# Kernel optimization log

Hardware: AMD Instinct MI355X
Metric: run time of the kernel (lower is better)

## Reference

```python
import jax, jax.numpy as jnp
import numpy as np

# 24 directional shifts (dy, dx): out[h,w] = in[h-dy, w-dx], zero elsewhere.
SHIFTS = [(0,1),(0,-1),(1,0),(-1,0),(1,1),(-1,-1),(1,-1),(-1,1),
          (0,2),(0,-2),(2,0),(-2,0),(2,2),(-2,-2),(2,-2),(-2,2),
          (2,1),(1,2),(2,-1),(1,-2),(-2,1),(-1,2),(-2,-1),(-1,-2)]

def shift2d(xg, dy, dx):
    B, G, H, W = xg.shape
    pt, pb = max(dy,0), max(-dy,0)
    pl, pr = max(dx,0), max(-dx,0)
    xp = jnp.pad(xg, ((0,0),(0,0),(pt,pb),(pl,pr)))
    return xp[:, :, pb:pb+H, pr:pr+W]

def mul_shift(x4, gamma=1.0/24.0):
    B, C, H, W = x4.shape
    g = int(C * gamma)
    parts = [shift2d(x4[:, i*g:(i+1)*g], dy, dx) for i, (dy, dx) in enumerate(SHIFTS)]
    parts.append(x4[:, 24*g:])
    return jnp.concatenate(parts, axis=1)

def zigzag_indices(h, w, start='top-left', direction='horizontal'):
    if start == 'top-left':   row_start, col_start, row_step, col_step = 0, 0, 1, 1
    elif start == 'top-right': row_start, col_start, row_step, col_step = 0, w-1, 1, -1
    elif start == 'bottom-left': row_start, col_start, row_step, col_step = h-1, 0, -1, 1
    else:                     row_start, col_start, row_step, col_step = h-1, w-1, -1, -1
    idx = []
    for i in range(h):
        r = row_start + row_step * i
        if direction == 'horizontal':
            cols = range(w) if r % 2 == 0 else range(w-1, -1, -1)
            idx += [r * w + c for c in cols]
        else:
            cc = col_start + col_step * i
            rows = range(h) if cc % 2 == 0 else range(h-1, -1, -1)
            idx += [rr * w + cc for rr in rows]
    return np.asarray(idx, dtype=np.int32)

def wkv(w, u, k, v):
    """Numerically stable RWKV WKV recurrence. w,u:(C,) k,v:(B,T,C) -> (B,T,C)."""
    B, T, C = k.shape
    def step(carry, kv):
        p, q, o = carry
        kt, vt = kv
        no = jnp.maximum(o, u + kt)
        A = jnp.exp(o - no); Bc = jnp.exp(u + kt - no)
        y = (A * p + Bc * vt) / (A * q + Bc)
        no2 = jnp.maximum(w + o, kt)
        A2 = jnp.exp(w + o - no2); B2 = jnp.exp(kt - no2)
        return (A2 * p + B2 * vt, A2 * q + B2, no2), y
    init = (jnp.zeros((B, C), k.dtype), jnp.zeros((B, C), k.dtype),
            jnp.full((B, C), -1e38, k.dtype))
    _, ys = jax.lax.scan(step, init, (jnp.swapaxes(k, 0, 1), jnp.swapaxes(v, 0, 1)))
    return jnp.swapaxes(ys, 0, 1)

def setup_inputs() -> dict:
    key = jax.random.key(0)
    ks = jax.random.split(key, 8)
    B, H, W, C = 8, 64, 64, 768
    scale = 0.02
    return {
        'x': jax.random.normal(ks[0], (B, H*W, C), jnp.float32),
        'key_w': jax.random.normal(ks[1], (C, C), jnp.float32) * scale,
        'value_w': jax.random.normal(ks[2], (C, C), jnp.float32) * scale,
        'receptance_w': jax.random.normal(ks[3], (C, C), jnp.float32) * scale,
        'output_w': jax.random.normal(ks[4], (C, C), jnp.float32) * scale,
        'spatial_decay': jax.random.normal(ks[5], (2, C), jnp.float32),
        'spatial_first': jax.random.normal(ks[6], (2, C), jnp.float32),
        'h': H, 'w': W,
    }

def reference(x, key_w, value_w, receptance_w, output_w, spatial_decay, spatial_first, h, w):
    B, T, C = x.shape
    # layer_id=0 -> scheme ('top-left','horizontal')
    order = jnp.asarray(zigzag_indices(h, w, 'top-left', 'horizontal'))
    inv = jnp.argsort(order)
    # jit_func: mul_shift in (B,C,H,W), zigzag reorder along T, projections
    x4 = jnp.transpose(x.reshape(B, h, w, C), (0, 3, 1, 2))
    x4 = mul_shift(x4)
    xs = jnp.transpose(x4.reshape(B, C, T)[:, :, order], (0, 2, 1))  # (B,T,C)
    k = xs @ key_w.T
    v = xs @ value_w.T
    sr = jax.nn.sigmoid(xs @ receptance_w.T)
    # recurrence j=0
    v = wkv(spatial_decay[0] / T, spatial_first[0] / T, k, v)
    # recurrence j=1: zigzag-permute, WKV, inverse-permute (horizontal -> same grid)
    k2 = k[:, order]
    v2 = v[:, order]
    v2 = wkv(spatial_decay[1] / T, spatial_first[1] / T, k2, v2)
    v = v2[:, inv]
    return (sr * v) @ output_w.T
```

## Files before the change

### kernel.cpp

```cpp
#include <hip/hip_runtime.h>
#include <hip/hip_bf16.h>
#include <hip/hip_fp16.h>

#define T_SEQ 4096
#define CDIM  768
#define BDIM  8
#define MROWS (BDIM * T_SEQ)
#define NKVR  (3 * CDIM)
#define CHL   32
#define NCH   (T_SEQ / CHL)
#define BC    (BDIM * CDIM)
#define BC2   (BC / 2)
#define CD2   (CDIM / 2)

typedef __attribute__((ext_vector_type(8))) short   short8;
typedef __attribute__((ext_vector_type(4))) float   floatx4;
typedef unsigned short ushort_t;
typedef unsigned int   uint_t;

__device__ __forceinline__ ushort_t f2b(float f) {
    __hip_bfloat16 h = __float2bfloat16(f);
    return *(ushort_t*)&h;
}
__device__ __forceinline__ float b2f(ushort_t s) {
    __hip_bfloat16 h;
    *(ushort_t*)&h = s;
    return __bfloat162float(h);
}
__device__ __forceinline__ ushort_t f2h(float f) {
    __half h = __float2half(f);
    return *(ushort_t*)&h;
}
__device__ __forceinline__ float h2f(ushort_t s) {
    __half h;
    *(ushort_t*)&h = s;
    return __half2float(h);
}

__device__ __forceinline__ void gload_lds16(const void* g, void* l) {
    __builtin_amdgcn_global_load_lds(
        (const __attribute__((address_space(1))) void*)g,
        (__attribute__((address_space(3))) void*)l, 16, 0, 0);
}

__constant__ int c_dy[24] = {0,0,1,-1,1,-1,1,-1,0,0,2,-2,2,-2,2,-2,2,1,2,1,-2,-1,-2,-1};
__constant__ int c_dx[24] = {1,-1,0,0,1,-1,-1,1,2,-2,0,0,2,-2,-2,2,1,2,-1,-2,1,2,-1,-2};

__global__ void cvt_weights(const float* __restrict__ kw, const float* __restrict__ vw,
                            const float* __restrict__ rw, const float* __restrict__ ow,
                            ushort_t* __restrict__ wkvr, ushort_t* __restrict__ wo) {
    int i = blockIdx.x * 256 + threadIdx.x;
    if (i < CDIM * CDIM) {
        wkvr[i]                   = f2b(kw[i]);
        wkvr[i + CDIM * CDIM]     = f2b(vw[i]);
        wkvr[i + 2 * CDIM * CDIM] = f2b(rw[i]);
        wo[i]                     = f2b(ow[i]);
    }
}

__global__ void shift_zigzag(const float* __restrict__ x, ushort_t* __restrict__ xs) {
    size_t i = (size_t)blockIdx.x * 256 + threadIdx.x;
    int c8 = (int)(i % (CDIM / 8)) * 8;
    size_t bt = i / (CDIM / 8);
    int tz = (int)(bt % T_SEQ);
    int b  = (int)(bt / T_SEQ);
    int r = tz >> 6, pos = tz & 63;
    int xcol = (r & 1) ? (63 - pos) : pos;
    int g = c8 >> 5;
    int ys = r - c_dy[g];
    int xsrc = xcol - c_dx[g];
    float4 v0 = {0.f, 0.f, 0.f, 0.f}, v1 = {0.f, 0.f, 0.f, 0.f};
    if ((unsigned)ys < 64u && (unsigned)xsrc < 64u) {
        const float* src = x + ((size_t)b * T_SEQ + (size_t)(ys * 64 + xsrc)) * CDIM + c8;
        v0 = *(const float4*)(src);
        v1 = *(const float4*)(src + 4);
    }
    short8 o;
    o[0] = (short)f2b(v0.x); o[1] = (short)f2b(v0.y);
    o[2] = (short)f2b(v0.z); o[3] = (short)f2b(v0.w);
    o[4] = (short)f2b(v1.x); o[5] = (short)f2b(v1.y);
    o[6] = (short)f2b(v1.z); o[7] = (short)f2b(v1.w);
    *(short8*)(xs + bt * CDIM + c8) = o;
}

template <int MODE, int NB>
__device__ __forceinline__ void gemm_body(
    const ushort_t* __restrict__ A, const ushort_t* __restrict__ Bw,
    ushort_t* __restrict__ kbuf, ushort_t* __restrict__ vbuf,
    ushort_t* __restrict__ out_sr, float* __restrict__ out_f) {
    __shared__ ushort_t As[128 * 64];
    __shared__ ushort_t Bs[128 * 64];
    const int p    = blockIdx.x;
    const int xcd  = p & 7;
    const int s    = p >> 3;
    const int mb   = xcd + 8 * (s / NB);
    const int nb   = s % NB;
    const int m0   = mb * 128;
    const int n0   = nb * 128;
    const int t    = threadIdx.x;
    const int lane = t & 63;
    const int wv   = t >> 6;
    const int wm   = (wv & 1) * 64;
    const int wn   = (wv >> 1) * 64;
    const int srow = t >> 3;
    const int sch  = t & 7;
    const int l15  = lane & 15;
    const int l4   = lane >> 4;

    floatx4 acc[4][4];
#pragma unroll
    for (int i = 0; i < 4; i++)
#pragma unroll
        for (int j = 0; j < 4; j++) acc[i][j] = (floatx4){0.f, 0.f, 0.f, 0.f};

    for (int kk = 0; kk < CDIM; kk += 64) {
        __syncthreads();
#pragma unroll
        for (int j = 0; j < 4; j++) {
            const int rowA = 32 * j + srow;
            const int gc   = sch ^ (rowA & 7);
            gload_lds16(A  + (size_t)(m0 + rowA) * CDIM + kk + gc * 8,
                        (void*)(As + j * 2048 + t * 8));
            gload_lds16(Bw + (size_t)(n0 + rowA) * CDIM + kk + gc * 8,
                        (void*)(Bs + j * 2048 + t * 8));
        }
        __syncthreads();
#pragma unroll
        for (int k2 = 0; k2 < 2; k2++) {
            short8 af[4], bfv[4];
#pragma unroll
            for (int mi = 0; mi < 4; mi++) {
                int ra = wm + mi * 16 + l15;
                int c  = k2 * 4 + l4;
                af[mi] = *(const short8*)(As + ra * 64 + ((c ^ (ra & 7)) << 3));
            }
#pragma unroll
            for (int ni = 0; ni < 4; ni++) {
                int rb = wn + ni * 16 + l15;
                int c  = k2 * 4 + l4;
                bfv[ni] = *(const short8*)(Bs + rb * 64 + ((c ^ (rb & 7)) << 3));
            }
#pragma unroll
            for (int mi = 0; mi < 4; mi++)
#pragma unroll
                for (int ni = 0; ni < 4; ni++)
                    acc[mi][ni] = __builtin_amdgcn_mfma_f32_16x16x32_bf16(
                        af[mi], bfv[ni], acc[mi][ni], 0, 0, 0);
        }
    }

    const int region = (MODE == 0) ? (nb / 6) : 0;
    const int ncb = n0 - region * CDIM;
#pragma unroll
    for (int mi = 0; mi < 4; mi++) {
#pragma unroll
        for (int ni = 0; ni < 4; ni++) {
            int nc = ncb + wn + ni * 16 + l15;
#pragma unroll
            for (int r = 0; r < 4; r++) {
                int mg = m0 + wm + mi * 16 + l4 * 4 + r;
                float val = acc[mi][ni][r];
                if (MODE == 0) {
                    if (region == 0)
                        kbuf[(size_t)mg * CDIM + nc] = f2h(val);
                    else if (region == 1)
                        vbuf[(size_t)mg * CDIM + nc] = f2h(val);
                    else
                        out_sr[(size_t)mg * CDIM + nc] =
                            f2b(1.0f / (1.0f + __expf(-val)));
                } else {
                    out_f[(size_t)mg * CDIM + (n0 + wn + ni * 16 + l15)] = val;
                }
            }
        }
    }
}

__global__ __launch_bounds__(256, 3) void gemm_kvr(
    const ushort_t* __restrict__ A, const ushort_t* __restrict__ Bw,
    ushort_t* __restrict__ kbuf, ushort_t* __restrict__ vbuf,
    ushort_t* __restrict__ out_sr) {
    gemm_body<0, 18>(A, Bw, kbuf, vbuf, out_sr, nullptr);
}

__global__ __launch_bounds__(256, 3) void gemm_out(
    const ushort_t* __restrict__ A, const ushort_t* __restrict__ Bw,
    float* __restrict__ out_f) {
    gemm_body<1, 6>(A, Bw, nullptr, nullptr, nullptr, out_f);
}


__global__ __launch_bounds__(256) void wkv_chunk_sum0(
    const ushort_t* __restrict__ kb, const ushort_t* __restrict__ vb,
    const float* __restrict__ sd,
    float* __restrict__ sumP, float* __restrict__ sumQ, float* __restrict__ sumO) {
    int gid = blockIdx.x * 256 + threadIdx.x;
    int bc2 = gid % BC2;
    int ch  = gid / BC2;
    int b = bc2 / CD2, cp = (bc2 % CD2) * 2;
    const float w0 = sd[cp]     * (1.0f / (float)T_SEQ);
    const float w1 = sd[cp + 1] * (1.0f / (float)T_SEQ);
    const size_t base = ((size_t)b * T_SEQ + ch * CHL) * CDIM + cp;
    const uint_t* kp = (const uint_t*)(kb + base);
    const uint_t* vp = (const uint_t*)(vb + base);
    float p0 = 0.f, q0 = 0.f, o0 = -1e38f;
    float p1 = 0.f, q1 = 0.f, o1 = -1e38f;
#pragma unroll 8
    for (int i = 0; i < CHL; i++) {
        uint_t ku = kp[(size_t)i * CD2], vu = vp[(size_t)i * CD2];
        float k0 = h2f((ushort_t)(ku & 0xffff)), k1 = h2f((ushort_t)(ku >> 16));
        float v0 = h2f((ushort_t)(vu & 0xffff)), v1 = h2f((ushort_t)(vu >> 16));
        float wo0 = w0 + o0, wo1 = w1 + o1;
        float n0_ = fmaxf(wo0, k0), n1_ = fmaxf(wo1, k1);
        float A0 = __expf(wo0 - n0_), B0 = __expf(k0 - n0_);
        float A1 = __expf(wo1 - n1_), B1 = __expf(k1 - n1_);
        p0 = A0 * p0 + B0 * v0;  q0 = A0 * q0 + B0;  o0 = n0_;
        p1 = A1 * p1 + B1 * v1;  q1 = A1 * q1 + B1;  o1 = n1_;
    }
    size_t idx = (size_t)ch * BC + (size_t)b * CDIM + cp;
    *(float2*)(sumP + idx) = make_float2(p0, p1);
    *(float2*)(sumQ + idx) = make_float2(q0, q1);
    *(float2*)(sumO + idx) = make_float2(o0, o1);
}

__global__ __launch_bounds__(256) void wkv_chunk_scan(
    const float* __restrict__ sumP, const float* __restrict__ sumQ,
    const float* __restrict__ sumO,
    float* __restrict__ inP, float* __restrict__ inQ, float* __restrict__ inO,
    const float* __restrict__ sd, int pass) {
    int bc = blockIdx.x * 256 + threadIdx.x;
    if (bc >= BC) return;
    int c = bc % CDIM;
    const float w = sd[pass * CDIM + c] * (1.0f / (float)T_SEQ);
    const float Lw = w * (float)CHL;
    float p = 0.f, q = 0.f, o = -1e38f;
#pragma unroll 4
    for (int ch = 0; ch < NCH; ch++) {
        size_t idx = (size_t)ch * BC + bc;
        inP[idx] = p; inQ[idx] = q; inO[idx] = o;
        float Pc = sumP[idx], Qc = sumQ[idx], Oc = sumO[idx];
        float ow_ = o + Lw;
        float no = fmaxf(ow_, Oc);
        float e1 = __expf(ow_ - no), e2 = __expf(Oc - no);
        p = e1 * p + e2 * Pc;
        q = e1 * q + e2 * Qc;
        o = no;
    }
}

__global__ __launch_bounds__(256) void wkv_replay0_sum1(
    const ushort_t* __restrict__ kb, ushort_t* __restrict__ vb,
    const float* __restrict__ sd, const float* __restrict__ sf,
    const float* __restrict__ inP, const float* __restrict__ inQ,
    const float* __restrict__ inO,
    float* __restrict__ sumP, float* __restrict__ sumQ, float* __restrict__ sumO) {
    int gid = blockIdx.x * 256 + threadIdx.x;
    int bc2 = gid % BC2;
    int ch  = gid / BC2;
    int b = bc2 / CD2, cp = (bc2 % CD2) * 2;
    const float w10 = sd[cp]     * (1.0f / (float)T_SEQ);
    const float w11 = sd[cp + 1] * (1.0f / (float)T_SEQ);
    const float u10 = sf[cp]     * (1.0f / (float)T_SEQ);
    const float u11 = sf[cp + 1] * (1.0f / (float)T_SEQ);
    const size_t base = ((size_t)b * T_SEQ + ch * CHL) * CDIM + cp;
    const uint_t* kp = (const uint_t*)(kb + base);
    uint_t* vp = (uint_t*)(vb + base);
    size_t idx = (size_t)ch * BC + (size_t)b * CDIM + cp;
    float2 pin = *(const float2*)(inP + idx);
    float2 qin = *(const float2*)(inQ + idx);
    float2 oin = *(const float2*)(inO + idx);
    float p0 = pin.x, q0 = qin.x, o0 = oin.x;
    float p1 = pin.y, q1 = qin.y, o1 = oin.y;
    uint_t ku_[CHL];
    uint_t yu_[CHL];
#pragma unroll
    for (int i = 0; i < CHL; i++) {
        uint_t ku = kp[(size_t)i * CD2];
        uint_t vu = vp[(size_t)i * CD2];
        ku_[i] = ku;
        float k0 = h2f((ushort_t)(ku & 0xffff)), k1 = h2f((ushort_t)(ku >> 16));
        float v0 = h2f((ushort_t)(vu & 0xffff)), v1 = h2f((ushort_t)(vu >> 16));
        float uk0 = u10 + k0;
        float no0 = fmaxf(o0, uk0);
        float Ae0 = __expf(o0 - no0), Be0 = __expf(uk0 - no0);
        float y0 = (Ae0 * p0 + Be0 * v0) / (Ae0 * q0 + Be0);
        float wo0 = w10 + o0;
        float nn0 = fmaxf(wo0, k0);
        float A20 = __expf(wo0 - nn0), B20 = __expf(k0 - nn0);
        p0 = A20 * p0 + B20 * v0;  q0 = A20 * q0 + B20;  o0 = nn0;
        float uk1 = u11 + k1;
        float no1 = fmaxf(o1, uk1);
        float Ae1 = __expf(o1 - no1), Be1 = __expf(uk1 - no1);
        float y1 = (Ae1 * p1 + Be1 * v1) / (Ae1 * q1 + Be1);
        float wo1 = w11 + o1;
        float nn1 = fmaxf(wo1, k1);
        float A21 = __expf(wo1 - nn1), B21 = __expf(k1 - nn1);
        p1 = A21 * p1 + B21 * v1;  q1 = A21 * q1 + B21;  o1 = nn1;
        uint_t yu = (uint_t)f2h(y0) | ((uint_t)f2h(y1) << 16);
        yu_[i] = yu;
        vp[(size_t)i * CD2] = yu;
    }
    const float w20 = sd[CDIM + cp]     * (1.0f / (float)T_SEQ);
    const float w21 = sd[CDIM + cp + 1] * (1.0f / (float)T_SEQ);
    float p20 = 0.f, q20 = 0.f, o20 = -1e38f;
    float p21 = 0.f, q21 = 0.f, o21 = -1e38f;
#define P2STEP(I)                                                              \
    {                                                                          \
        uint_t ku = ku_[(I)], yu = yu_[(I)];                                   \
        float k0 = h2f((ushort_t)(ku & 0xffff)), k1 = h2f((ushort_t)(ku >> 16)); \
        float y0 = h2f((ushort_t)(yu & 0xffff)), y1 = h2f((ushort_t)(yu >> 16)); \
        float wo0 = w20 + o20, wo1 = w21 + o21;                                \
        float nn0 = fmaxf(wo0, k0), nn1 = fmaxf(wo1, k1);                      \
        float A20 = __expf(wo0 - nn0), B20 = __expf(k0 - nn0);                 \
        float A21 = __expf(wo1 - nn1), B21 = __expf(k1 - nn1);                 \
        p20 = A20 * p20 + B20 * y0;  q20 = A20 * q20 + B20;  o20 = nn0;        \
        p21 = A21 * p21 + B21 * y1;  q21 = A21 * q21 + B21;  o21 = nn1;        \
    }
    if (((ch >> 1) & 1) == 0) {
#pragma unroll
        for (int j = 0; j < CHL; j++) P2STEP(j)
    } else {
#pragma unroll
        for (int j = 0; j < CHL; j++) P2STEP(CHL - 1 - j)
    }
#undef P2STEP
    size_t idx2 = (size_t)((ch & 2) ? (ch ^ 1) : ch) * BC + (size_t)b * CDIM + cp;
    *(float2*)(sumP + idx2) = make_float2(p20, p21);
    *(float2*)(sumQ + idx2) = make_float2(q20, q21);
    *(float2*)(sumO + idx2) = make_float2(o20, o21);
}

__global__ __launch_bounds__(256) void wkv_replay1(
    const ushort_t* __restrict__ kb, const ushort_t* __restrict__ vb,
    const ushort_t* __restrict__ srb, ushort_t* __restrict__ a2,
    const float* __restrict__ sd, const float* __restrict__ sf,
    const float* __restrict__ inP, const float* __restrict__ inQ,
    const float* __restrict__ inO) {
    int gid = blockIdx.x * 256 + threadIdx.x;
    int bc2 = gid % BC2;
    int ch  = gid / BC2;
    int b = bc2 / CD2, cp = (bc2 % CD2) * 2;
    const float w0 = sd[CDIM + cp]     * (1.0f / (float)T_SEQ);
    const float w1 = sd[CDIM + cp + 1] * (1.0f / (float)T_SEQ);
    const float u0 = sf[CDIM + cp]     * (1.0f / (float)T_SEQ);
    const float u1 = sf[CDIM + cp + 1] * (1.0f / (float)T_SEQ);
    size_t base = (size_t)b * T_SEQ * CDIM + cp;
    size_t idx = (size_t)ch * BC + (size_t)b * CDIM + cp;
    float2 pin = *(const float2*)(inP + idx);
    float2 qin = *(const float2*)(inQ + idx);
    float2 oin = *(const float2*)(inO + idx);
    float p0 = pin.x, q0 = qin.x, o0 = oin.x;
    float p1 = pin.y, q1 = qin.y, o1 = oin.y;
    const int r = ch >> 1;
    const int pos0 = (ch & 1) * CHL;
#pragma unroll 8
    for (int i = 0; i < CHL; i++) {
        int pos = pos0 + i;
        int col = (r & 1) ? (63 - pos) : pos;
        size_t off = base + (size_t)(r * 64 + col) * CDIM;
        uint_t ku = *(const uint_t*)(kb + off);
        uint_t vu = *(const uint_t*)(vb + off);
        uint_t su = *(const uint_t*)(srb + off);
        float k0 = h2f((ushort_t)(ku & 0xffff)), k1 = h2f((ushort_t)(ku >> 16));
        float v0 = h2f((ushort_t)(vu & 0xffff)), v1 = h2f((ushort_t)(vu >> 16));
        float uk0 = u0 + k0;
        float no0 = fmaxf(o0, uk0);
        float Ae0 = __expf(o0 - no0), Be0 = __expf(uk0 - no0);
        float y0 = (Ae0 * p0 + Be0 * v0) / (Ae0 * q0 + Be0);
        float wo0 = w0 + o0;
        float nn0 = fmaxf(wo0, k0);
        float A20 = __expf(wo0 - nn0), B20 = __expf(k0 - nn0);
        p0 = A20 * p0 + B20 * v0;  q0 = A20 * q0 + B20;  o0 = nn0;
        float uk1 = u1 + k1;
        float no1 = fmaxf(o1, uk1);
        float Ae1 = __expf(o1 - no1), Be1 = __expf(uk1 - no1);
        float y1 = (Ae1 * p1 + Be1 * v1) / (Ae1 * q1 + Be1);
        float wo1 = w1 + o1;
        float nn1 = fmaxf(wo1, k1);
        float A21 = __expf(wo1 - nn1), B21 = __expf(k1 - nn1);
        p1 = A21 * p1 + B21 * v1;  q1 = A21 * q1 + B21;  o1 = nn1;
        uint_t out = (uint_t)f2b(y0 * b2f((ushort_t)(su & 0xffff))) |
                     ((uint_t)f2b(y1 * b2f((ushort_t)(su >> 16))) << 16);
        *(uint_t*)(a2 + off) = out;
    }
}

extern "C" void kernel_launch(void* const* d_in, const int* in_sizes, int n_in,
                              void* d_out, int out_size, void* d_ws, size_t ws_size,
                              hipStream_t stream) {
    (void)in_sizes; (void)n_in; (void)out_size; (void)ws_size;
    const float* x  = (const float*)d_in[0];
    const float* kw = (const float*)d_in[1];
    const float* vw = (const float*)d_in[2];
    const float* rw = (const float*)d_in[3];
    const float* ow = (const float*)d_in[4];
    const float* sd = (const float*)d_in[5];
    const float* sf = (const float*)d_in[6];
    float* out = (float*)d_out;

    char* ws = (char*)d_ws;
    size_t off = 0;
    auto alloc = [&](size_t bytes) -> void* {
        void* p = ws + off;
        off += (bytes + 255) & ~(size_t)255;
        return p;
    };
    ushort_t* xs   = (ushort_t*)alloc((size_t)MROWS * CDIM * 2);
    ushort_t* kb   = (ushort_t*)alloc((size_t)MROWS * CDIM * 2);
    ushort_t* vb   = (ushort_t*)alloc((size_t)MROWS * CDIM * 2);
    ushort_t* srb  = (ushort_t*)alloc((size_t)MROWS * CDIM * 2);
    ushort_t* wkvr = (ushort_t*)alloc((size_t)NKVR * CDIM * 2);
    ushort_t* wo   = (ushort_t*)alloc((size_t)CDIM * CDIM * 2);
    float*    sumP = (float*)   alloc((size_t)NCH * BC * 4);
    float*    sumQ = (float*)   alloc((size_t)NCH * BC * 4);
    float*    sumO = (float*)   alloc((size_t)NCH * BC * 4);
    float*    inP  = (float*)   alloc((size_t)NCH * BC * 4);
    float*    inQ  = (float*)   alloc((size_t)NCH * BC * 4);
    float*    inO  = (float*)   alloc((size_t)NCH * BC * 4);

    cvt_weights<<<(CDIM * CDIM + 255) / 256, 256, 0, stream>>>(kw, vw, rw, ow, wkvr, wo);
    shift_zigzag<<<(int)((size_t)MROWS * (CDIM / 8) / 256), 256, 0, stream>>>(x, xs);
    gemm_kvr<<<(MROWS / 128) * (NKVR / 128), 256, 0, stream>>>(
        xs, wkvr, kb, vb, srb);

    const int nwkv2 = NCH * BC2;
    wkv_chunk_sum0<<<nwkv2 / 256, 256, 0, stream>>>(kb, vb, sd, sumP, sumQ, sumO);
    wkv_chunk_scan<<<(BC + 255) / 256, 256, 0, stream>>>(sumP, sumQ, sumO,
                                                         inP, inQ, inO, sd, 0);
    wkv_replay0_sum1<<<nwkv2 / 256, 256, 0, stream>>>(kb, vb, sd, sf,
                                                      inP, inQ, inO, sumP, sumQ, sumO);
    wkv_chunk_scan<<<(BC + 255) / 256, 256, 0, stream>>>(sumP, sumQ, sumO,
                                                         inP, inQ, inO, sd, 1);
    wkv_replay1<<<nwkv2 / 256, 256, 0, stream>>>(kb, vb, srb, xs,
                                                 sd, sf, inP, inQ, inO);

    gemm_out<<<(MROWS / 128) * (CDIM / 128), 256, 0, stream>>>(xs, wo, out);
}
```

Measured before the change: 523.1 us.

## Double-buffer GEMM LDS tiles with K=32 stages and prefetch

The GEMM main loop moves from one 64-wide K tile per iteration with two barriers to double-buffered 32-wide K tiles. The next tile's global-to-LDS loads are issued before the current tile's MFMAs, and only one barrier runs per iteration. The aim is to overlap memory latency with matrix math and cut synchronisation stalls. The cost is twice as many loop iterations, each doing half the MFMA work, plus a new XOR swizzle for the narrower rows that may change LDS bank-conflict behaviour.

```diff
diff --git a/kernel.cpp b/kernel.cpp
--- a/kernel.cpp
+++ b/kernel.cpp
@@ -12,6 +12,7 @@
 #define BC    (BDIM * CDIM)
 #define BC2   (BC / 2)
 #define CD2   (CDIM / 2)
+#define NKT32 (CDIM / 32)
 
 typedef __attribute__((ext_vector_type(8))) short   short8;
 typedef __attribute__((ext_vector_type(4))) float   floatx4;
@@ -88,8 +89,8 @@
     const ushort_t* __restrict__ A, const ushort_t* __restrict__ Bw,
     ushort_t* __restrict__ kbuf, ushort_t* __restrict__ vbuf,
     ushort_t* __restrict__ out_sr, float* __restrict__ out_f) {
-    __shared__ ushort_t As[128 * 64];
-    __shared__ ushort_t Bs[128 * 64];
+    __shared__ ushort_t As[2][128 * 32];
+    __shared__ ushort_t Bs[2][128 * 32];
     const int p    = blockIdx.x;
     const int xcd  = p & 7;
     const int s    = p >> 3;
@@ -102,52 +103,62 @@
     const int wv   = t >> 6;
     const int wm   = (wv & 1) * 64;
     const int wn   = (wv >> 1) * 64;
-    const int srow = t >> 3;
-    const int sch  = t & 7;
     const int l15  = lane & 15;
     const int l4   = lane >> 4;
 
+    const int ci0 = t;
+    const int r0  = ci0 >> 2, s0 = ci0 & 3;
+    const int ci1 = t + 256;
+    const int r1  = ci1 >> 2, s1 = ci1 & 3;
+    const int gc0 = s0 ^ ((r0 >> 1) & 3);
+    const int gc1 = s1 ^ ((r1 >> 1) & 3);
+
     floatx4 acc[4][4];
 #pragma unroll
     for (int i = 0; i < 4; i++)
 #pragma unroll
         for (int j = 0; j < 4; j++) acc[i][j] = (floatx4){0.f, 0.f, 0.f, 0.f};
 
-    for (int kk = 0; kk < CDIM; kk += 64) {
+#define STAGE32(BUF, KK)                                                     \
+    {                                                                        \
+        gload_lds16(A  + (size_t)(m0 + r0) * CDIM + (KK) + gc0 * 8,          \
+                    (void*)(&As[(BUF)][0] + ci0 * 8));                       \
+        gload_lds16(A  + (size_t)(m0 + r1) * CDIM + (KK) + gc1 * 8,          \
+                    (void*)(&As[(BUF)][0] + ci1 * 8));                       \
+        gload_lds16(Bw + (size_t)(n0 + r0) * CDIM + (KK) + gc0 * 8,          \
+                    (void*)(&Bs[(BUF)][0] + ci0 * 8));                       \
+        gload_lds16(Bw + (size_t)(n0 + r1) * CDIM + (KK) + gc1 * 8,          \
+                    (void*)(&Bs[(BUF)][0] + ci1 * 8));                       \
+    }
+
+    STAGE32(0, 0)
+    __syncthreads();
+
+    for (int kt = 0; kt < NKT32; kt++) {
+        const int cur = kt & 1;
+        if (kt + 1 < NKT32) STAGE32(cur ^ 1, (kt + 1) * 32)
+        short8 af[4], bfv[4];
+#pragma unroll
+        for (int mi = 0; mi < 4; mi++) {
+            int ra = wm + mi * 16 + l15;
+            af[mi] = *(const short8*)(&As[cur][0] + ra * 32 +
+                                      ((l4 ^ ((ra >> 1) & 3)) << 3));
+        }
+#pragma unroll
+        for (int ni = 0; ni < 4; ni++) {
+            int rb = wn + ni * 16 + l15;
+            bfv[ni] = *(const short8*)(&Bs[cur][0] + rb * 32 +
+                                       ((l4 ^ ((rb >> 1) & 3)) << 3));
+        }
+#pragma unroll
+        for (int mi = 0; mi < 4; mi++)
+#pragma unroll
+            for (int ni = 0; ni < 4; ni++)
+                acc[mi][ni] = __builtin_amdgcn_mfma_f32_16x16x32_bf16(
+                    af[mi], bfv[ni], acc[mi][ni], 0, 0, 0);
         __syncthreads();
-#pragma unroll
-        for (int j = 0; j < 4; j++) {
-            const int rowA = 32 * j + srow;
-            const int gc   = sch ^ (rowA & 7);
-            gload_lds16(A  + (size_t)(m0 + rowA) * CDIM + kk + gc * 8,
-                        (void*)(As + j * 2048 + t * 8));
-            gload_lds16(Bw + (size_t)(n0 + rowA) * CDIM + kk + gc * 8,
-                        (void*)(Bs + j * 2048 + t * 8));
-        }
-        __syncthreads();
-#pragma unroll
-        for (int k2 = 0; k2 < 2; k2++) {
-            short8 af[4], bfv[4];
-#pragma unroll
-            for (int mi = 0; mi < 4; mi++) {
-                int ra = wm + mi * 16 + l15;
-                int c  = k2 * 4 + l4;
-                af[mi] = *(const short8*)(As + ra * 64 + ((c ^ (ra & 7)) << 3));
-            }
-#pragma unroll
-            for (int ni = 0; ni < 4; ni++) {
-                int rb = wn + ni * 16 + l15;
-                int c  = k2 * 4 + l4;
-                bfv[ni] = *(const short8*)(Bs + rb * 64 + ((c ^ (rb & 7)) << 3));
-            }
-#pragma unroll
-            for (int mi = 0; mi < 4; mi++)
-#pragma unroll
-                for (int ni = 0; ni < 4; ni++)
-                    acc[mi][ni] = __builtin_amdgcn_mfma_f32_16x16x32_bf16(
-                        af[mi], bfv[ni], acc[mi][ni], 0, 0, 0);
-        }
-    }
+    }
+#undef STAGE32
 
     const int region = (MODE == 0) ? (nb / 6) : 0;
     const int ncb = n0 - region * CDIM;
```

Measured after the change: 552.0 us. 1.06x slower.
